# Optimization experiments

Hardware: AMD Instinct MI355X
Metric: run time of the kernel (lower is better)

## Reference

```python
import jax, jax.numpy as jnp
import numpy as np

EPS = 1e-12
ALPHA = 0.2  # LeakyReLU negative slope
N_NODES = 100000
N_EDGES = 1600000
F = 128
H = 8

def setup_inputs() -> dict:
    key = jax.random.key(0)
    k1, k2, k3, k4 = jax.random.split(key, 4)
    x = jax.random.normal(k1, (N_NODES, F), dtype=jnp.float32)
    row = jax.random.randint(k2, (N_EDGES,), 0, N_NODES, dtype=jnp.int32)
    col = jax.random.randint(k3, (N_EDGES,), 0, N_NODES, dtype=jnp.int32)
    # xavier_uniform with gain=1.414 on [H, 2F]
    limit = 1.414 * np.sqrt(6.0 / (H + 2 * F))
    aa = jax.random.uniform(k4, (H, 2 * F), dtype=jnp.float32, minval=-limit, maxval=limit)
    return {"x": x, "row": row, "col": col, "aa": aa}

def reference(x, row, col, aa):
    # e = leakyrelu(aa @ cat(x[row], x[col], dim=1).T)  -> [H, E]
    # Split aa so per-node scores are computed once, then gathered per edge
    # (identical math, avoids materializing the [E, 2F] concat).
    a_src, a_dst = aa[:, :F], aa[:, F:]          # [H, F] each
    s_src = x @ a_src.T                           # [N, H]
    s_dst = x @ a_dst.T                           # [N, H]
    e = s_src[row] + s_dst[col]                   # [E, H]
    e = jnp.where(e > 0, e, ALPHA * e)            # LeakyReLU
    # scatter_softmax over edges grouped by row (per head)
    m = jax.ops.segment_max(e, row, num_segments=N_NODES)  # [N, H]
    m = jnp.where(jnp.isfinite(m), m, 0.0)        # empty segments -> -inf; neutralize
    ex = jnp.exp(e - m[row])                      # [E, H]
    s = jax.ops.segment_sum(ex, row, num_segments=N_NODES)  # [N, H]
    a = ex / (s[row] + EPS)                       # [E, H]
    return a.T                                    # [H, E] to match torch layout
```

## Files before the change

### kernel.cpp

```cpp
#include <hip/hip_runtime.h>

constexpr int N_NODES = 100000;
constexpr int N_EDGES = 1600000;
constexpr int F = 128;
constexpr int H = 8;
constexpr float ALPHA = 0.2f;
constexpr float EPSF = 1e-12f;

constexpr int PSHIFT = 8;
constexpr int PN = 1 << PSHIFT;
constexpr int NPART = (N_NODES + PN - 1) / PN;
constexpr int MAXPART = 5120;
constexpr int EPB = 4096;
constexpr int OCAP = 4096;

__global__ void k1_scores(const float* __restrict__ x, const float* __restrict__ aa,
                          float* __restrict__ srn, float* __restrict__ s_dst) {
    __shared__ float sa[H * 2 * F];
    for (int i = threadIdx.x; i < H * 2 * F; i += blockDim.x) sa[i] = aa[i];
    __syncthreads();
    int node = blockIdx.x * blockDim.x + threadIdx.x;
    if (node >= N_NODES) return;
    const float4* xr = reinterpret_cast<const float4*>(x + (size_t)node * F);
    float accs[H], accd[H];
#pragma unroll
    for (int h = 0; h < H; ++h) { accs[h] = 0.f; accd[h] = 0.f; }
    for (int f4 = 0; f4 < F / 4; ++f4) {
        float4 xv = xr[f4];
#pragma unroll
        for (int h = 0; h < H; ++h) {
            float4 av = *reinterpret_cast<const float4*>(&sa[h * 2 * F + 4 * f4]);
            float4 bv = *reinterpret_cast<const float4*>(&sa[h * 2 * F + F + 4 * f4]);
            accs[h] += xv.x * av.x + xv.y * av.y + xv.z * av.z + xv.w * av.w;
            accd[h] += xv.x * bv.x + xv.y * bv.y + xv.z * bv.z + xv.w * bv.w;
        }
    }
    float4* os = reinterpret_cast<float4*>(srn + (size_t)node * 16);
    os[0] = make_float4(accs[0], accs[1], accs[2], accs[3]);
    os[1] = make_float4(accs[4], accs[5], accs[6], accs[7]);
    float4* od = reinterpret_cast<float4*>(s_dst + (size_t)node * H);
    od[0] = make_float4(accd[0], accd[1], accd[2], accd[3]);
    od[1] = make_float4(accd[4], accd[5], accd[6], accd[7]);
}

__global__ void __launch_bounds__(1024)
kA_part(const int* __restrict__ row, const int* __restrict__ col,
        int* __restrict__ gcnt, unsigned* __restrict__ part,
        int* __restrict__ ocnt, int2* __restrict__ olist) {
    __shared__ int hist[NPART];
    __shared__ int base[NPART];
    const int t = threadIdx.x;
    const int e0 = blockIdx.x * EPB;
    for (int p = t; p < NPART; p += 1024) hist[p] = 0;
    __syncthreads();
    for (int k = 0; k < EPB / 1024; ++k) {
        int i = e0 + k * 1024 + t;
        if (i < N_EDGES) atomicAdd(&hist[row[i] >> PSHIFT], 1);
    }
    __syncthreads();
    for (int p = t; p < NPART; p += 1024) {
        int h = hist[p];
        base[p] = h ? atomicAdd(&gcnt[p], h) : 0;
        hist[p] = 0;
    }
    __syncthreads();
    for (int k = 0; k < EPB / 1024; ++k) {
        int i = e0 + k * 1024 + t;
        if (i < N_EDGES) {
            int r = row[i], c = col[i];
            int p = r >> PSHIFT;
            int slot = base[p] + atomicAdd(&hist[p], 1);
            unsigned pk = ((unsigned)(r & (PN - 1)) << 17) | (unsigned)c;
            if (slot < MAXPART) {
                part[(size_t)p * MAXPART + slot] = pk;
            } else {
                int q = atomicAdd(ocnt, 1);
                if (q < OCAP) olist[q] = make_int2(p, (int)pk);
            }
        }
    }
}

__global__ void __launch_bounds__(1024)
kB_sum(const float* __restrict__ s_dst, const unsigned* __restrict__ part,
       const int* __restrict__ gcnt, const int* __restrict__ ocnt,
       const int2* __restrict__ olist, float* __restrict__ srn) {
    __shared__ unsigned plist[MAXPART];
    __shared__ unsigned sorted_c[MAXPART];
    __shared__ int hist[PN];
    __shared__ int off[PN + 1];
    __shared__ int cur[PN];
    const int p = blockIdx.x;
    const int t = threadIdx.x;
    const int nbase = p << PSHIFT;

    for (int i = t; i < PN; i += 1024) hist[i] = 0;
    __syncthreads();

    int cnt = gcnt[p]; if (cnt > MAXPART) cnt = MAXPART;
    const unsigned* pp = part + (size_t)p * MAXPART;

    for (int i = t; i < cnt; i += 1024) {
        unsigned pk = pp[i];
        plist[i] = pk;
        atomicAdd(&hist[pk >> 17], 1);
    }
    __syncthreads();

    for (int d = 1; d < PN; d <<= 1) {
        int add = 0;
        if (t >= d && t < PN) add = hist[t - d];
        __syncthreads();
        if (t < PN) hist[t] += add;
        __syncthreads();
    }
    if (t < PN) off[t + 1] = hist[t];
    if (t == 0) off[0] = 0;
    __syncthreads();
    if (t < PN) cur[t] = off[t];
    __syncthreads();

    for (int i = t; i < cnt; i += 1024) {
        unsigned pk = plist[i];
        int rl = (int)(pk >> 17);
        int slot = atomicAdd(&cur[rl], 1);
        sorted_c[slot] = pk & 0x1FFFFu;
    }
    __syncthreads();

    int mo = *ocnt; if (mo > OCAP) mo = OCAP;
    for (int pair = t; pair < PN * H; pair += 1024) {
        int nl = pair >> 3, h = pair & 7;
        int node = nbase + nl;
        int k0 = off[nl], k1 = off[nl + 1];
        float s = (node < N_NODES) ? srn[(size_t)node * 16 + h] : 0.f;
        float a = 0.f;
        for (int k = k0; k < k1; ++k) {
            int c = (int)sorted_c[k];
            float e = s + s_dst[(size_t)c * H + h];
            e = e > 0.f ? e : ALPHA * e;
            a += __expf(e);
        }
        if (mo > 0) {
            for (int j = 0; j < mo; ++j) {
                int2 oe = olist[j];
                if (oe.x == p && (int)(((unsigned)oe.y) >> 17) == nl) {
                    int c = oe.y & 0x1FFFF;
                    float e = s + s_dst[(size_t)c * H + h];
                    e = e > 0.f ? e : ALPHA * e;
                    a += __expf(e);
                }
            }
        }
        if (node < N_NODES) srn[(size_t)node * 16 + 8 + h] = 1.0f / (a + EPSF);
    }
}

__global__ void k4_out(const int* __restrict__ row, const int* __restrict__ col,
                       const float* __restrict__ srn, const float* __restrict__ s_dst,
                       float* __restrict__ out) {
    int i = blockIdx.x * blockDim.x + threadIdx.x;
    if (i >= N_EDGES) return;
    int r = row[i], c = col[i];
    const float4* sr = reinterpret_cast<const float4*>(srn + (size_t)r * 16);
    float4 a0 = sr[0], a1 = sr[1], r0 = sr[2], r1 = sr[3];
    const float4* sc = reinterpret_cast<const float4*>(s_dst + (size_t)c * H);
    float4 b0 = sc[0], b1 = sc[1];
    float ev[H] = {a0.x + b0.x, a0.y + b0.y, a0.z + b0.z, a0.w + b0.w,
                   a1.x + b1.x, a1.y + b1.y, a1.z + b1.z, a1.w + b1.w};
    float rv[H] = {r0.x, r0.y, r0.z, r0.w, r1.x, r1.y, r1.z, r1.w};
#pragma unroll
    for (int h = 0; h < H; ++h) {
        float e = ev[h] > 0.f ? ev[h] : ALPHA * ev[h];
        out[(size_t)h * N_EDGES + i] = __expf(e) * rv[h];
    }
}

__global__ void kz_zero_sums(float* __restrict__ srn) {
    int t = blockIdx.x * blockDim.x + threadIdx.x;
    if (t >= N_NODES * H) return;
    srn[(size_t)(t >> 3) * 16 + 8 + (t & 7)] = 0.f;
}

__global__ void k3nm_sum(const float* __restrict__ srn_ro, const float* __restrict__ s_dst,
                         const int* __restrict__ row, const int* __restrict__ col,
                         float* __restrict__ srn) {
    int i = blockIdx.x * blockDim.x + threadIdx.x;
    if (i >= N_EDGES) return;
    int r = row[i], c = col[i];
    const float4* sr = reinterpret_cast<const float4*>(srn_ro + (size_t)r * 16);
    float4 a0 = sr[0], a1 = sr[1];
    const float4* sc = reinterpret_cast<const float4*>(s_dst + (size_t)c * H);
    float4 b0 = sc[0], b1 = sc[1];
    float ev[H] = {a0.x + b0.x, a0.y + b0.y, a0.z + b0.z, a0.w + b0.w,
                   a1.x + b1.x, a1.y + b1.y, a1.z + b1.z, a1.w + b1.w};
#pragma unroll
    for (int h = 0; h < H; ++h) {
        float e = ev[h] > 0.f ? ev[h] : ALPHA * ev[h];
        atomicAdd(&srn[(size_t)r * 16 + 8 + h], __expf(e));
    }
}

__global__ void k_inv(float* __restrict__ srn) {
    int t = blockIdx.x * blockDim.x + threadIdx.x;
    if (t >= N_NODES * H) return;
    int n = t >> 3, h = t & 7;
    float s = srn[(size_t)n * 16 + 8 + h];
    srn[(size_t)n * 16 + 8 + h] = 1.0f / (s + EPSF);
}

extern "C" void kernel_launch(void* const* d_in, const int* in_sizes, int n_in,
                              void* d_out, int out_size, void* d_ws, size_t ws_size,
                              hipStream_t stream) {
    const float* x   = (const float*)d_in[0];
    const int*   row = (const int*)d_in[1];
    const int*   col = (const int*)d_in[2];
    const float* aa  = (const float*)d_in[3];
    float* out = (float*)d_out;

    float*    srn   = (float*)d_ws;
    float*    s_dst = srn + (size_t)N_NODES * 16;
    unsigned* part  = (unsigned*)(s_dst + (size_t)N_NODES * H);
    int*      gcnt  = (int*)(part + (size_t)NPART * MAXPART);
    int*      ocnt  = gcnt + NPART;
    int2*     olist = (int2*)(ocnt + 16);

    const size_t need_b = ((size_t)N_NODES * 24 + (size_t)NPART * MAXPART
                           + NPART + 16 + 2 * OCAP) * 4;

    const int B = 256;
    const int GE = (N_EDGES + B - 1) / B;
    const int GN = (N_NODES + B - 1) / B;

    k1_scores<<<GN, B, 0, stream>>>(x, aa, srn, s_dst);

    if (ws_size >= need_b) {
        hipMemsetAsync(gcnt, 0, (size_t)(NPART + 16) * sizeof(int), stream);
        kA_part<<<(N_EDGES + EPB - 1) / EPB, 1024, 0, stream>>>(row, col, gcnt, part, ocnt, olist);
        kB_sum<<<NPART, 1024, 0, stream>>>(s_dst, part, gcnt, ocnt, olist, srn);
    } else {
        kz_zero_sums<<<(N_NODES * H + B - 1) / B, B, 0, stream>>>(srn);
        k3nm_sum<<<GE, B, 0, stream>>>(srn, s_dst, row, col, srn);
        k_inv<<<(N_NODES * H + B - 1) / B, B, 0, stream>>>(srn);
    }

    k4_out<<<GE, B, 0, stream>>>(row, col, srn, s_dst, out);
}
```

Before: 220.1 us.

## Split per-node scores into head-pair planes for gather locality in output kernel

k1 also writes s_dst as head-pair planes (float2 per node per pair). kB_sum stages the source scores in shared memory, processes two heads per thread, and writes a per-pair float4 plane {s_src pair, inverse sums pair}. A new k4p kernel runs a 2D grid over (edges, head pair) and gathers compact 8- and 16-byte records per pair instead of 48 bytes per edge, so each pass has a smaller random-access working set that fits better in cache. In exchange, row and col are read four times, and extra workspace plus extra writes in k1 are needed.

Result: no change. 222.6 us (+1.1%).

```diff
diff --git a/kernel.cpp b/kernel.cpp
--- a/kernel.cpp
+++ b/kernel.cpp
@@ -13,9 +13,11 @@
 constexpr int MAXPART = 5120;
 constexpr int EPB = 4096;
 constexpr int OCAP = 4096;
+constexpr int NPAIR = H / 2;
 
 __global__ void k1_scores(const float* __restrict__ x, const float* __restrict__ aa,
-                          float* __restrict__ srn, float* __restrict__ s_dst) {
+                          float* __restrict__ srn, float* __restrict__ sd,
+                          float2* __restrict__ sd2) {
     __shared__ float sa[H * 2 * F];
     for (int i = threadIdx.x; i < H * 2 * F; i += blockDim.x) sa[i] = aa[i];
     __syncthreads();
@@ -38,9 +40,12 @@
     float4* os = reinterpret_cast<float4*>(srn + (size_t)node * 16);
     os[0] = make_float4(accs[0], accs[1], accs[2], accs[3]);
     os[1] = make_float4(accs[4], accs[5], accs[6], accs[7]);
-    float4* od = reinterpret_cast<float4*>(s_dst + (size_t)node * H);
+    float4* od = reinterpret_cast<float4*>(sd + (size_t)node * H);
     od[0] = make_float4(accd[0], accd[1], accd[2], accd[3]);
     od[1] = make_float4(accd[4], accd[5], accd[6], accd[7]);
+#pragma unroll
+    for (int pi = 0; pi < NPAIR; ++pi)
+        sd2[(size_t)pi * N_NODES + node] = make_float2(accd[2 * pi], accd[2 * pi + 1]);
 }
 
 __global__ void __launch_bounds__(1024)
@@ -82,19 +87,25 @@
 }
 
 __global__ void __launch_bounds__(1024)
-kB_sum(const float* __restrict__ s_dst, const unsigned* __restrict__ part,
+kB_sum(const float* __restrict__ sd, const unsigned* __restrict__ part,
        const int* __restrict__ gcnt, const int* __restrict__ ocnt,
-       const int2* __restrict__ olist, float* __restrict__ srn) {
+       const int2* __restrict__ olist, const float* __restrict__ srn,
+       float4* __restrict__ spn) {
     __shared__ unsigned plist[MAXPART];
     __shared__ unsigned sorted_c[MAXPART];
     __shared__ int hist[PN];
     __shared__ int off[PN + 1];
     __shared__ int cur[PN];
+    __shared__ float ssrc[PN * H];
     const int p = blockIdx.x;
     const int t = threadIdx.x;
     const int nbase = p << PSHIFT;
 
     for (int i = t; i < PN; i += 1024) hist[i] = 0;
+    for (int j = t; j < PN * H; j += 1024) {
+        int n = nbase + (j >> 3);
+        ssrc[j] = (n < N_NODES) ? srn[(size_t)n * 16 + (j & 7)] : 0.f;
+    }
     __syncthreads();
 
     int cnt = gcnt[p]; if (cnt > MAXPART) cnt = MAXPART;
@@ -129,31 +140,82 @@
     __syncthreads();
 
     int mo = *ocnt; if (mo > OCAP) mo = OCAP;
-    for (int pair = t; pair < PN * H; pair += 1024) {
-        int nl = pair >> 3, h = pair & 7;
+    {
+        int nl = t >> 2, pi = t & 3;
         int node = nbase + nl;
-        int k0 = off[nl], k1 = off[nl + 1];
-        float s = (node < N_NODES) ? srn[(size_t)node * 16 + h] : 0.f;
-        float a = 0.f;
-        for (int k = k0; k < k1; ++k) {
+        int k0 = off[nl], k1e = off[nl + 1];
+        float s0 = ssrc[nl * 8 + 2 * pi];
+        float s1 = ssrc[nl * 8 + 2 * pi + 1];
+        float a0 = 0.f, a1 = 0.f;
+        for (int k = k0; k < k1e; ++k) {
             int c = (int)sorted_c[k];
-            float e = s + s_dst[(size_t)c * H + h];
-            e = e > 0.f ? e : ALPHA * e;
-            a += __expf(e);
-        }
-        if (mo > 0) {
-            for (int j = 0; j < mo; ++j) {
-                int2 oe = olist[j];
-                if (oe.x == p && (int)(((unsigned)oe.y) >> 17) == nl) {
-                    int c = oe.y & 0x1FFFF;
-                    float e = s + s_dst[(size_t)c * H + h];
-                    e = e > 0.f ? e : ALPHA * e;
-                    a += __expf(e);
-                }
+            float2 d = *reinterpret_cast<const float2*>(&sd[(size_t)c * H + 2 * pi]);
+            float e0 = s0 + d.x; e0 = e0 > 0.f ? e0 : ALPHA * e0;
+            float e1 = s1 + d.y; e1 = e1 > 0.f ? e1 : ALPHA * e1;
+            a0 += __expf(e0); a1 += __expf(e1);
+        }
+        for (int j = 0; j < mo; ++j) {
+            int2 oe = olist[j];
+            if (oe.x == p && (int)(((unsigned)oe.y) >> 17) == nl) {
+                int c = oe.y & 0x1FFFF;
+                float2 d = *reinterpret_cast<const float2*>(&sd[(size_t)c * H + 2 * pi]);
+                float e0 = s0 + d.x; e0 = e0 > 0.f ? e0 : ALPHA * e0;
+                float e1 = s1 + d.y; e1 = e1 > 0.f ? e1 : ALPHA * e1;
+                a0 += __expf(e0); a1 += __expf(e1);
             }
         }
-        if (node < N_NODES) srn[(size_t)node * 16 + 8 + h] = 1.0f / (a + EPSF);
-    }
+        if (node < N_NODES)
+            spn[(size_t)pi * N_NODES + node] =
+                make_float4(s0, s1, 1.f / (a0 + EPSF), 1.f / (a1 + EPSF));
+    }
+}
+
+__global__ void k4p(const int* __restrict__ row, const int* __restrict__ col,
+                    const float4* __restrict__ spn, const float2* __restrict__ sd2,
+                    float* __restrict__ out) {
+    int i = blockIdx.x * blockDim.x + threadIdx.x;
+    if (i >= N_EDGES) return;
+    int pi = blockIdx.y;
+    int r = row[i], c = col[i];
+    float4 q = spn[(size_t)pi * N_NODES + r];
+    float2 d = sd2[(size_t)pi * N_NODES + c];
+    float e0 = q.x + d.x; e0 = e0 > 0.f ? e0 : ALPHA * e0;
+    float e1 = q.y + d.y; e1 = e1 > 0.f ? e1 : ALPHA * e1;
+    out[(size_t)(2 * pi) * N_EDGES + i]     = __expf(e0) * q.z;
+    out[(size_t)(2 * pi + 1) * N_EDGES + i] = __expf(e1) * q.w;
+}
+
+__global__ void kz_zero_sums(float* __restrict__ srn) {
+    int t = blockIdx.x * blockDim.x + threadIdx.x;
+    if (t >= N_NODES * H) return;
+    srn[(size_t)(t >> 3) * 16 + 8 + (t & 7)] = 0.f;
+}
+
+__global__ void k3nm_sum(const float* __restrict__ srn_ro, const float* __restrict__ s_dst,
+                         const int* __restrict__ row, const int* __restrict__ col,
+                         float* __restrict__ srn) {
+    int i = blockIdx.x * blockDim.x + threadIdx.x;
+    if (i >= N_EDGES) return;
+    int r = row[i], c = col[i];
+    const float4* sr = reinterpret_cast<const float4*>(srn_ro + (size_t)r * 16);
+    float4 a0 = sr[0], a1 = sr[1];
+    const float4* sc = reinterpret_cast<const float4*>(s_dst + (size_t)c * H);
+    float4 b0 = sc[0], b1 = sc[1];
+    float ev[H] = {a0.x + b0.x, a0.y + b0.y, a0.z + b0.z, a0.w + b0.w,
+                   a1.x + b1.x, a1.y + b1.y, a1.z + b1.z, a1.w + b1.w};
+#pragma unroll
+    for (int h = 0; h < H; ++h) {
+        float e = ev[h] > 0.f ? ev[h] : ALPHA * ev[h];
+        atomicAdd(&srn[(size_t)r * 16 + 8 + h], __expf(e));
+    }
+}
+
+__global__ void k_inv(float* __restrict__ srn) {
+    int t = blockIdx.x * blockDim.x + threadIdx.x;
+    if (t >= N_NODES * H) return;
+    int n = t >> 3, h = t & 7;
+    float s = srn[(size_t)n * 16 + 8 + h];
+    srn[(size_t)n * 16 + 8 + h] = 1.0f / (s + EPSF);
 }
 
 __global__ void k4_out(const int* __restrict__ row, const int* __restrict__ col,
@@ -176,39 +238,6 @@
     }
 }
 
-__global__ void kz_zero_sums(float* __restrict__ srn) {
-    int t = blockIdx.x * blockDim.x + threadIdx.x;
-    if (t >= N_NODES * H) return;
-    srn[(size_t)(t >> 3) * 16 + 8 + (t & 7)] = 0.f;
-}
-
-__global__ void k3nm_sum(const float* __restrict__ srn_ro, const float* __restrict__ s_dst,
-                         const int* __restrict__ row, const int* __restrict__ col,
-                         float* __restrict__ srn) {
-    int i = blockIdx.x * blockDim.x + threadIdx.x;
-    if (i >= N_EDGES) return;
-    int r = row[i], c = col[i];
-    const float4* sr = reinterpret_cast<const float4*>(srn_ro + (size_t)r * 16);
-    float4 a0 = sr[0], a1 = sr[1];
-    const float4* sc = reinterpret_cast<const float4*>(s_dst + (size_t)c * H);
-    float4 b0 = sc[0], b1 = sc[1];
-    float ev[H] = {a0.x + b0.x, a0.y + b0.y, a0.z + b0.z, a0.w + b0.w,
-                   a1.x + b1.x, a1.y + b1.y, a1.z + b1.z, a1.w + b1.w};
-#pragma unroll
-    for (int h = 0; h < H; ++h) {
-        float e = ev[h] > 0.f ? ev[h] : ALPHA * ev[h];
-        atomicAdd(&srn[(size_t)r * 16 + 8 + h], __expf(e));
-    }
-}
-
-__global__ void k_inv(float* __restrict__ srn) {
-    int t = blockIdx.x * blockDim.x + threadIdx.x;
-    if (t >= N_NODES * H) return;
-    int n = t >> 3, h = t & 7;
-    float s = srn[(size_t)n * 16 + 8 + h];
-    srn[(size_t)n * 16 + 8 + h] = 1.0f / (s + EPSF);
-}
-
 extern "C" void kernel_launch(void* const* d_in, const int* in_sizes, int n_in,
                               void* d_out, int out_size, void* d_ws, size_t ws_size,
                               hipStream_t stream) {
@@ -218,31 +247,35 @@
     const float* aa  = (const float*)d_in[3];
     float* out = (float*)d_out;
 
-    float*    srn   = (float*)d_ws;
-    float*    s_dst = srn + (size_t)N_NODES * 16;
-    unsigned* part  = (unsigned*)(s_dst + (size_t)N_NODES * H);
-    int*      gcnt  = (int*)(part + (size_t)NPART * MAXPART);
-    int*      ocnt  = gcnt + NPART;
+    float*    srn  = (float*)d_ws;
+    float*    sd   = srn + (size_t)N_NODES * 16;
+    float4*   spn  = (float4*)(sd + (size_t)N_NODES * H);
+    float2*   sd2  = (float2*)(spn + (size_t)NPAIR * N_NODES);
+    unsigned* part = (unsigned*)(sd2 + (size_t)NPAIR * N_NODES);
+    int*      gcnt = (int*)(part + (size_t)NPART * MAXPART);
+    int*      ocnt = gcnt + NPART;
     int2*     olist = (int2*)(ocnt + 16);
 
-    const size_t need_b = ((size_t)N_NODES * 24 + (size_t)NPART * MAXPART
-                           + NPART + 16 + 2 * OCAP) * 4;
+    const size_t need_full = ((size_t)N_NODES * (16 + 8 + 16 + 8) + (size_t)NPART * MAXPART
+                              + NPART + 16 + 2 * OCAP) * 4;
+    const size_t need_min  = (size_t)N_NODES * (16 + 8) * 4;
 
     const int B = 256;
     const int GE = (N_EDGES + B - 1) / B;
     const int GN = (N_NODES + B - 1) / B;
 
-    k1_scores<<<GN, B, 0, stream>>>(x, aa, srn, s_dst);
-
-    if (ws_size >= need_b) {
+    k1_scores<<<GN, B, 0, stream>>>(x, aa, srn, sd, sd2);
+
+    if (ws_size >= need_full) {
         hipMemsetAsync(gcnt, 0, (size_t)(NPART + 16) * sizeof(int), stream);
         kA_part<<<(N_EDGES + EPB - 1) / EPB, 1024, 0, stream>>>(row, col, gcnt, part, ocnt, olist);
-        kB_sum<<<NPART, 1024, 0, stream>>>(s_dst, part, gcnt, ocnt, olist, srn);
-    } else {
+        kB_sum<<<NPART, 1024, 0, stream>>>(sd, part, gcnt, ocnt, olist, srn, spn);
+        dim3 g4(GE, NPAIR);
+        k4p<<<g4, B, 0, stream>>>(row, col, spn, sd2, out);
+    } else if (ws_size >= need_min) {
         kz_zero_sums<<<(N_NODES * H + B - 1) / B, B, 0, stream>>>(srn);
-        k3nm_sum<<<GE, B, 0, stream>>>(srn, s_dst, row, col, srn);
+        k3nm_sum<<<GE, B, 0, stream>>>(srn, sd, row, col, srn);
         k_inv<<<(N_NODES * H + B - 1) / B, B, 0, stream>>>(srn);
-    }
-
-    k4_out<<<GE, B, 0, stream>>>(row, col, srn, s_dst, out);
-}
+        k4_out<<<GE, B, 0, stream>>>(row, col, srn, sd, out);
+    }
+}
```
